# Performance work log

Hardware: AMD Instinct MI355X
Metric: run time of the kernel (lower is better)

## Reference

```python
import jax, jax.numpy as jnp
import numpy as np

NX, DX, H, DO = 8192, 8, 1024, 1


def setup_inputs() -> dict:
    key = jax.random.key(0)
    ks = jax.random.split(key, 7)
    s1 = 1.0 / np.sqrt(DX)  # torch Linear default init bound
    s2 = 1.0 / np.sqrt(H)
    x = jax.random.normal(ks[0], (NX, DX), jnp.float32)
    W1 = jax.random.uniform(ks[1], (H, DX), jnp.float32, -s1, s1)
    b1 = jax.random.uniform(ks[2], (H,), jnp.float32, -s1, s1)
    W2 = jax.random.uniform(ks[3], (H, H), jnp.float32, -s2, s2)
    b2 = jax.random.uniform(ks[4], (H,), jnp.float32, -s2, s2)
    W3 = jax.random.uniform(ks[5], (DO, H), jnp.float32, -s2, s2)
    b3 = jax.random.uniform(ks[6], (DO,), jnp.float32, -s2, s2)
    return {"x": x, "W1": W1, "b1": b1, "W2": W2, "b2": b2, "W3": W3, "b3": b3}


def reference(x, W1, b1, W2, b2, W3, b3):
    # Forward: Linear -> Tanh -> Linear -> Tanh -> Linear
    z1 = jnp.tanh(x @ W1.T + b1)          # [nx, h]
    z2 = jnp.tanh(z1 @ W2.T + b2)         # [nx, h]
    y = z2 @ W3.T + b3                    # [nx, out]

    # DerivTanh(h) = 4/(e^-h + e^h)^2 = sech^2(h) = 1 - tanh(h)^2
    d1 = 1.0 - z1 * z1                    # [nx, h]
    d2 = 1.0 - z2 * z2                    # [nx, h]

    # Vectorized analytic Jacobian (original loops over each input dim k):
    # tmp_k = d2 * (W2 @ (d1 * W1[:, k]))  then  dydx_k = W3 @ tmp_k
    J = d1[:, :, None] * W1[None, :, :]                    # [nx, h, dx]
    J = d2[:, :, None] * jnp.einsum('ij,njk->nik', W2, J)  # [nx, h, dx]
    dydx = jnp.einsum('oj,njk->nok', W3, J)                # [nx, out, dx]
    # Match original list-of-dx ordering: dydx[k] has shape [nx, out]
    dydx = jnp.transpose(dydx, (2, 0, 1))                  # [dx, nx, out]
    return y, dydx
```

## Files before the change

kernel.cpp:

```cpp
#include <hip/hip_runtime.h>
#include <stdint.h>

#define NXS 8192
#define HS  1024

typedef __attribute__((ext_vector_type(8))) short short8;
typedef __attribute__((ext_vector_type(4))) float f32x4;

__device__ __forceinline__ float bf2f(uint32_t b) {
    union { uint32_t u; float f; } c; c.u = b << 16; return c.f;
}
__device__ __forceinline__ uint16_t f2bf(float f) {
    union { float f; uint32_t u; } c; c.f = f;
    return (uint16_t)((c.u + 0x7fffu + ((c.u >> 16) & 1u)) >> 16);
}


__global__ __launch_bounds__(256) void k01(
    const float* __restrict__ x, const float* __restrict__ W1,
    const float* __restrict__ b1, const float* __restrict__ W2,
    const float* __restrict__ b3, uint16_t* __restrict__ Z1p,
    uint16_t* __restrict__ Bp1, uint16_t* __restrict__ Bp2,
    uint16_t* __restrict__ W1T, float* __restrict__ out)
{
    const int b = blockIdx.x, t = threadIdx.x;
    if (b < 512) {
        __shared__ float w1s[8192];
        __shared__ float b1s[1024];
        __shared__ float xs[16][8];
        const int rt = b;
#pragma unroll
        for (int i = 0; i < 8; ++i)
            *(float4*)&w1s[(i * 256 + t) * 4] = *(const float4*)(W1 + (i * 256 + t) * 4);
#pragma unroll
        for (int i = 0; i < 4; ++i) b1s[i * 256 + t] = b1[i * 256 + t];
        if (t < 128) xs[t >> 3][t & 7] = x[rt * 128 + t];
        __syncthreads();
        const int r = t & 15;
        float xv[8];
#pragma unroll
        for (int k = 0; k < 8; ++k) xv[k] = xs[r][k];
#pragma unroll
        for (int c8 = 0; c8 < 8; ++c8) {
            const int kb = (t >> 4) + c8 * 16;
            uint16_t o[8];
#pragma unroll
            for (int j = 0; j < 8; ++j) {
                const int col = kb * 8 + j;
                float s = b1s[col];
#pragma unroll
                for (int k = 0; k < 8; ++k) s += xv[k] * w1s[col * 8 + k];
                o[j] = f2bf(tanhf(s));
            }
            const int c = kb >> 2, lq = kb & 3;
            uint16_t* dst = Z1p + ((size_t)(rt * 32 + c) * 64 + lq * 16 + r) * 8;
            *(ushort4*)dst       = *(ushort4*)&o[0];
            *(ushort4*)(dst + 4) = *(ushort4*)&o[4];
        }
    } else if (b < 1024) {
        const int tid = (b - 512) * 256 + t;
        const int l = tid & 63, c = (tid >> 6) & 31, g = tid >> 11;
        const int lr = l & 15, lq = l >> 4;
        const float* src = W2 + (size_t)(g * 16 + lr) * HS + c * 32 + lq * 8;
        float4 a0 = *(const float4*)src;
        float4 a1 = *(const float4*)(src + 4);
        uint16_t o[8];
        o[0] = f2bf(a0.x); o[1] = f2bf(a0.y); o[2] = f2bf(a0.z); o[3] = f2bf(a0.w);
        o[4] = f2bf(a1.x); o[5] = f2bf(a1.y); o[6] = f2bf(a1.z); o[7] = f2bf(a1.w);
        *(ushort4*)(Bp1 + (size_t)tid * 8)     = *(ushort4*)&o[0];
        *(ushort4*)(Bp1 + (size_t)tid * 8 + 4) = *(ushort4*)&o[4];
    } else if (b < 1536) {
        const int tid = (b - 1024) * 256 + t;
        const int l = tid & 63, c = (tid >> 6) & 31, g = tid >> 11;
        const int lr = l & 15, lq = l >> 4;
        uint16_t o[8];
#pragma unroll
        for (int j2 = 0; j2 < 8; ++j2)
            o[j2] = f2bf(W2[(size_t)(c * 32 + lq * 8 + j2) * HS + g * 16 + lr]);
        *(ushort4*)(Bp2 + (size_t)tid * 8)     = *(ushort4*)&o[0];
        *(ushort4*)(Bp2 + (size_t)tid * 8 + 4) = *(ushort4*)&o[4];
    } else if (b < 1824) {
        const int idx = (b - 1536) * 256 + t;
        out[idx] = (idx < NXS) ? b3[0] : 0.f;
    } else {
        const int idx = (b - 1824) * 256 + t;
        const int r = idx >> 10, cc = idx & 1023;
        W1T[idx] = (r < 8) ? f2bf(W1[cc * 8 + r]) : (uint16_t)0;
    }
}

template <int MODE>
__global__ __launch_bounds__(256, 4) void gemm_k(
    const uint16_t* __restrict__ Ap, const uint16_t* __restrict__ Bp,
    const float* __restrict__ bias, const float* __restrict__ W3,
    uint16_t* __restrict__ Vp, float* __restrict__ yOut,
    const uint16_t* __restrict__ Z1p, const uint16_t* __restrict__ W1T,
    float* __restrict__ dOut)
{
    __shared__ __attribute__((aligned(16))) uint16_t smem[64 * 136];
    const int t = threadIdx.x;
    const int wave = t >> 6, lane = t & 63;
    const int lq = lane >> 4, lr = lane & 15;
    const int rowBase = blockIdx.x * 64;
    const int colBase = blockIdx.y * 128;

    const uint16_t* pA  = Ap + ((size_t)(rowBase >> 4) * 32) * 512 + (size_t)lane * 8;
    const uint16_t* pB0 = Bp + ((size_t)(colBase >> 4) + wave * 2) * 16384 + (size_t)lane * 8;
    const uint16_t* pB1 = pB0 + 16384;

    f32x4 acc[4][2] = {};

    short8 ac[4], b0c, b1c;
#pragma unroll
    for (int ti = 0; ti < 4; ++ti)
        ac[ti] = *(const short8*)(pA + (size_t)ti * 16384);
    b0c = *(const short8*)pB0;
    b1c = *(const short8*)pB1;

    for (int c = 0; c < 32; ++c) {
        short8 an[4] = {ac[0], ac[1], ac[2], ac[3]};
        short8 b0n = b0c, b1n = b1c;
        if (c < 31) {
            const size_t off = (size_t)(c + 1) * 512;
#pragma unroll
            for (int ti = 0; ti < 4; ++ti)
                an[ti] = *(const short8*)(pA + (size_t)ti * 16384 + off);
            b0n = *(const short8*)(pB0 + off);
            b1n = *(const short8*)(pB1 + off);
        }
#pragma unroll
        for (int ti = 0; ti < 4; ++ti) {
            acc[ti][0] = __builtin_amdgcn_mfma_f32_16x16x32_bf16(ac[ti], b0c, acc[ti][0], 0, 0, 0);
            acc[ti][1] = __builtin_amdgcn_mfma_f32_16x16x32_bf16(ac[ti], b1c, acc[ti][1], 0, 0, 0);
        }
#pragma unroll
        for (int ti = 0; ti < 4; ++ti) ac[ti] = an[ti];
        b0c = b0n; b1c = b1n;
    }

    if (MODE == 0) {
        float cB[2], cW[2]; int cCol[2];
#pragma unroll
        for (int tj = 0; tj < 2; ++tj) {
            cCol[tj] = wave * 32 + tj * 16 + lr;
            cB[tj] = bias[colBase + cCol[tj]];
            cW[tj] = W3[colBase + cCol[tj]];
        }
#pragma unroll
        for (int ti = 0; ti < 4; ++ti) {
#pragma unroll
            for (int r = 0; r < 4; ++r) {
                int rowl = ti * 16 + lq * 4 + r;
                float ys = 0.f;
#pragma unroll
                for (int tj = 0; tj < 2; ++tj) {
                    float z2 = tanhf(acc[ti][tj][r] + cB[tj]);
                    ys += z2 * cW[tj];
                    smem[rowl * 136 + cCol[tj]] = f2bf((1.f - z2 * z2) * cW[tj]);
                }
                ys += __shfl_xor(ys, 1); ys += __shfl_xor(ys, 2);
                ys += __shfl_xor(ys, 4); ys += __shfl_xor(ys, 8);
                if (lr == 0) atomicAdd(&yOut[rowBase + rowl], ys);
            }
        }
        __syncthreads();
#pragma unroll
        for (int i = 0; i < 4; ++i) {
            const int s = i * 256 + t;
            const int rl = s >> 4, kc = s & 15;
            short8 v = *(const short8*)(smem + rl * 136 + kc * 8);
            const int rt = (rowBase >> 4) + (rl >> 4);
            const int c2 = (colBase >> 5) + (kc >> 2);
            *(short8*)(Vp + ((size_t)(rt * 32 + c2) * 64 + (kc & 3) * 16 + (rl & 15)) * 8) = v;
        }
    } else {
#pragma unroll
        for (int ti = 0; ti < 4; ++ti)
#pragma unroll
            for (int r = 0; r < 4; ++r) {
                const int rowl = ti * 16 + lq * 4 + r;
                const int rt_z = (rowBase >> 4) + ti;
                const int lrp = lq * 4 + r;
#pragma unroll
                for (int tj = 0; tj < 2; ++tj) {
                    const int col = colBase + wave * 32 + tj * 16 + lr;
                    const int cz = col >> 5, lqz = (col >> 3) & 3, jz = col & 7;
                    float z1 = bf2f(Z1p[((size_t)(rt_z * 32 + cz) * 64 + lqz * 16 + lrp) * 8 + jz]);
                    smem[rowl * 136 + wave * 32 + tj * 16 + lr] =
                        f2bf(acc[ti][tj][r] * (1.f - z1 * z1));
                }
            }
        __syncthreads();
        f32x4 dd = {};
#pragma unroll
        for (int kb = 0; kb < 4; ++kb) {
            short8 aF = *(const short8*)(smem + (wave * 16 + lr) * 136 + kb * 32 + lq * 8);
            short8 bF = *(const short8*)(W1T + lr * HS + colBase + kb * 32 + lq * 8);
            dd = __builtin_amdgcn_mfma_f32_16x16x32_bf16(aF, bF, dd, 0, 0, 0);
        }
        if (lr < 8) {
            const int row = rowBase + wave * 16 + lq * 4;
#pragma unroll
            for (int rg = 0; rg < 4; ++rg)
                atomicAdd(&dOut[(size_t)lr * NXS + row + rg], dd[rg]);
        }
    }
}

extern "C" void kernel_launch(void* const* d_in, const int* in_sizes, int n_in,
                              void* d_out, int out_size, void* d_ws, size_t ws_size,
                              hipStream_t stream) {
    (void)in_sizes; (void)n_in; (void)out_size; (void)ws_size;
    const float* x  = (const float*)d_in[0];
    const float* W1 = (const float*)d_in[1];
    const float* b1 = (const float*)d_in[2];
    const float* W2 = (const float*)d_in[3];
    const float* b2 = (const float*)d_in[4];
    const float* W3 = (const float*)d_in[5];
    const float* b3 = (const float*)d_in[6];
    float* out = (float*)d_out;

    char* ws = (char*)d_ws;
    uint16_t* Z1p = (uint16_t*)(ws);
    uint16_t* Vp  = (uint16_t*)(ws + (size_t)16 * 1024 * 1024);
    uint16_t* Bp1 = (uint16_t*)(ws + (size_t)32 * 1024 * 1024);
    uint16_t* Bp2 = (uint16_t*)(ws + (size_t)34 * 1024 * 1024);
    uint16_t* W1T = (uint16_t*)(ws + (size_t)36 * 1024 * 1024);

    k01<<<1888, 256, 0, stream>>>(x, W1, b1, W2, b3, Z1p, Bp1, Bp2, W1T, out);
    gemm_k<0><<<dim3(NXS / 64, HS / 128), 256, 0, stream>>>(
        Z1p, Bp1, b2, W3, Vp, out, nullptr, nullptr, nullptr);
    gemm_k<1><<<dim3(NXS / 64, HS / 128), 256, 0, stream>>>(
        Vp, Bp2, nullptr, nullptr, nullptr, nullptr, Z1p, W1T, out + NXS);
}
```

Before: 154.1 us.

## Stage A tiles through LDS with async global-to-LDS triple buffering

The A operand is no longer loaded redundantly by each of the four waves straight from global memory. Each block now copies it once per step into a three-slot LDS ring using global_load_lds, which all waves then read. The B fragments stay in registers with two k-chunks prefetched per iteration, and there is one barrier per iteration. This cuts A global traffic roughly fourfold at the cost of LDS reads and a sync each step. The ring reuse depends on barrier ordering and async-copy completion, which is a correctness risk.

```diff
diff --git a/kernel.cpp b/kernel.cpp
--- a/kernel.cpp
+++ b/kernel.cpp
@@ -13,6 +13,12 @@
 __device__ __forceinline__ uint16_t f2bf(float f) {
     union { float f; uint32_t u; } c; c.f = f;
     return (uint16_t)((c.u + 0x7fffu + ((c.u >> 16) & 1u)) >> 16);
+}
+__device__ __forceinline__ void async_cp16(const void* g, void* l) {
+    __builtin_amdgcn_global_load_lds(
+        (const __attribute__((address_space(1))) void*)g,
+        (__attribute__((address_space(3))) void*)l,
+        16, 0, 0);
 }
 
 
@@ -97,46 +103,62 @@
     const uint16_t* __restrict__ Z1p, const uint16_t* __restrict__ W1T,
     float* __restrict__ dOut)
 {
-    __shared__ __attribute__((aligned(16))) uint16_t smem[64 * 136];
+    __shared__ __attribute__((aligned(16))) uint16_t smem[12288];
     const int t = threadIdx.x;
     const int wave = t >> 6, lane = t & 63;
     const int lq = lane >> 4, lr = lane & 15;
     const int rowBase = blockIdx.x * 64;
     const int colBase = blockIdx.y * 128;
 
-    const uint16_t* pA  = Ap + ((size_t)(rowBase >> 4) * 32) * 512 + (size_t)lane * 8;
+    const int ti0 = t >> 7, cp = (t >> 6) & 1, ln = t & 63;
+    const uint16_t* gA0 = Ap + (((size_t)(rowBase >> 4) + ti0) * 32 + cp) * 512 + (size_t)ln * 8;
+    const uint16_t* gA1 = Ap + (((size_t)(rowBase >> 4) + ti0 + 2) * 32 + cp) * 512 + (size_t)ln * 8;
     const uint16_t* pB0 = Bp + ((size_t)(colBase >> 4) + wave * 2) * 16384 + (size_t)lane * 8;
     const uint16_t* pB1 = pB0 + 16384;
 
     f32x4 acc[4][2] = {};
 
-    short8 ac[4], b0c, b1c;
-#pragma unroll
-    for (int ti = 0; ti < 4; ++ti)
-        ac[ti] = *(const short8*)(pA + (size_t)ti * 16384);
-    b0c = *(const short8*)pB0;
-    b1c = *(const short8*)pB1;
-
-    for (int c = 0; c < 32; ++c) {
-        short8 an[4] = {ac[0], ac[1], ac[2], ac[3]};
-        short8 b0n = b0c, b1n = b1c;
-        if (c < 31) {
-            const size_t off = (size_t)(c + 1) * 512;
+    async_cp16(gA0, (char*)smem + t * 16);
+    async_cp16(gA1, (char*)smem + 4096 + t * 16);
+    short8 bc00 = *(const short8*)pB0;
+    short8 bc01 = *(const short8*)pB1;
+    short8 bc10 = *(const short8*)(pB0 + 512);
+    short8 bc11 = *(const short8*)(pB1 + 512);
+
+    int buf = 0;
+    for (int it = 0; it < 16; ++it) {
+        short8 bn00 = bc00, bn01 = bc01, bn10 = bc10, bn11 = bc11;
+        const int nb = (buf == 2) ? 0 : buf + 1;
+        if (it < 15) {
+            const size_t aoff = (size_t)(it + 1) * 1024;
+            async_cp16(gA0 + aoff, (char*)smem + nb * 8192 + t * 16);
+            async_cp16(gA1 + aoff, (char*)smem + nb * 8192 + 4096 + t * 16);
+            const size_t boff = (size_t)(2 * it + 2) * 512;
+            bn00 = *(const short8*)(pB0 + boff);
+            bn01 = *(const short8*)(pB1 + boff);
+            bn10 = *(const short8*)(pB0 + boff + 512);
+            bn11 = *(const short8*)(pB1 + boff + 512);
+        }
+        __syncthreads();
+        const short* pA = (const short*)smem + buf * 4096;
+#pragma unroll
+        for (int kk = 0; kk < 2; ++kk) {
+            short8 af[4];
 #pragma unroll
             for (int ti = 0; ti < 4; ++ti)
-                an[ti] = *(const short8*)(pA + (size_t)ti * 16384 + off);
-            b0n = *(const short8*)(pB0 + off);
-            b1n = *(const short8*)(pB1 + off);
-        }
-#pragma unroll
-        for (int ti = 0; ti < 4; ++ti) {
-            acc[ti][0] = __builtin_amdgcn_mfma_f32_16x16x32_bf16(ac[ti], b0c, acc[ti][0], 0, 0, 0);
-            acc[ti][1] = __builtin_amdgcn_mfma_f32_16x16x32_bf16(ac[ti], b1c, acc[ti][1], 0, 0, 0);
-        }
-#pragma unroll
-        for (int ti = 0; ti < 4; ++ti) ac[ti] = an[ti];
-        b0c = b0n; b1c = b1n;
+                af[ti] = *(const short8*)(pA + ti * 1024 + kk * 512 + lane * 8);
+            const short8 b0 = kk ? bc10 : bc00;
+            const short8 b1 = kk ? bc11 : bc01;
+#pragma unroll
+            for (int ti = 0; ti < 4; ++ti) {
+                acc[ti][0] = __builtin_amdgcn_mfma_f32_16x16x32_bf16(af[ti], b0, acc[ti][0], 0, 0, 0);
+                acc[ti][1] = __builtin_amdgcn_mfma_f32_16x16x32_bf16(af[ti], b1, acc[ti][1], 0, 0, 0);
+            }
+        }
+        bc00 = bn00; bc01 = bn01; bc10 = bn10; bc11 = bn11;
+        buf = nb;
     }
+    __syncthreads();
 
     if (MODE == 0) {
         float cB[2], cW[2]; int cCol[2];
```

Result: faster. 137.0 us (-11.1%).

## Stage A tiles in LDS via async copy with 2x2 wave layout

Applied to the files above, without the earlier changes.

The GEMM main loop now loads the shared A row-tile into LDS once per block, using global_load_lds async copies in a triple-buffered ring. Previously every wave read all four A fragments from global memory itself. Waves are rearranged into a 2x2 grid, each computing a 32x64 sub-tile, so A fragments are reused from LDS and each wave reads four B fragments. This cuts redundant global A traffic but adds a __syncthreads per K iteration and more B register pressure.

```diff
diff --git a/kernel.cpp b/kernel.cpp
--- a/kernel.cpp
+++ b/kernel.cpp
@@ -13,6 +13,12 @@
 __device__ __forceinline__ uint16_t f2bf(float f) {
     union { float f; uint32_t u; } c; c.f = f;
     return (uint16_t)((c.u + 0x7fffu + ((c.u >> 16) & 1u)) >> 16);
+}
+__device__ __forceinline__ void async_cp16(const void* g, void* l) {
+    __builtin_amdgcn_global_load_lds(
+        (const __attribute__((address_space(1))) void*)g,
+        (__attribute__((address_space(3))) void*)l,
+        16, 0, 0);
 }
 
 
@@ -97,63 +103,73 @@
     const uint16_t* __restrict__ Z1p, const uint16_t* __restrict__ W1T,
     float* __restrict__ dOut)
 {
-    __shared__ __attribute__((aligned(16))) uint16_t smem[64 * 136];
+    __shared__ __attribute__((aligned(16))) uint16_t smem[8704];
     const int t = threadIdx.x;
     const int wave = t >> 6, lane = t & 63;
     const int lq = lane >> 4, lr = lane & 15;
+    const int wm = wave >> 1, wn = wave & 1;
     const int rowBase = blockIdx.x * 64;
     const int colBase = blockIdx.y * 128;
 
-    const uint16_t* pA  = Ap + ((size_t)(rowBase >> 4) * 32) * 512 + (size_t)lane * 8;
-    const uint16_t* pB0 = Bp + ((size_t)(colBase >> 4) + wave * 2) * 16384 + (size_t)lane * 8;
-    const uint16_t* pB1 = pB0 + 16384;
-
-    f32x4 acc[4][2] = {};
-
-    short8 ac[4], b0c, b1c;
-#pragma unroll
-    for (int ti = 0; ti < 4; ++ti)
-        ac[ti] = *(const short8*)(pA + (size_t)ti * 16384);
-    b0c = *(const short8*)pB0;
-    b1c = *(const short8*)pB1;
-
-    for (int c = 0; c < 32; ++c) {
-        short8 an[4] = {ac[0], ac[1], ac[2], ac[3]};
-        short8 b0n = b0c, b1n = b1c;
-        if (c < 31) {
-            const size_t off = (size_t)(c + 1) * 512;
-#pragma unroll
-            for (int ti = 0; ti < 4; ++ti)
-                an[ti] = *(const short8*)(pA + (size_t)ti * 16384 + off);
-            b0n = *(const short8*)(pB0 + off);
-            b1n = *(const short8*)(pB1 + off);
-        }
-#pragma unroll
-        for (int ti = 0; ti < 4; ++ti) {
-            acc[ti][0] = __builtin_amdgcn_mfma_f32_16x16x32_bf16(ac[ti], b0c, acc[ti][0], 0, 0, 0);
-            acc[ti][1] = __builtin_amdgcn_mfma_f32_16x16x32_bf16(ac[ti], b1c, acc[ti][1], 0, 0, 0);
-        }
-#pragma unroll
-        for (int ti = 0; ti < 4; ++ti) ac[ti] = an[ti];
-        b0c = b0n; b1c = b1n;
+    const uint16_t* gA = Ap + ((size_t)((rowBase >> 4) + (t >> 6)) * 32) * 512
+                            + (size_t)(t & 63) * 8;
+    const uint16_t* pB[4];
+#pragma unroll
+    for (int tj = 0; tj < 4; ++tj)
+        pB[tj] = Bp + ((size_t)(colBase >> 4) + wn * 4 + tj) * 16384 + (size_t)lane * 8;
+
+    f32x4 acc[2][4] = {};
+
+    async_cp16(gA, (char*)smem + t * 16);
+    short8 bc[4];
+#pragma unroll
+    for (int tj = 0; tj < 4; ++tj) bc[tj] = *(const short8*)pB[tj];
+
+    int buf = 0;
+    for (int it = 0; it < 32; ++it) {
+        short8 bn[4] = {bc[0], bc[1], bc[2], bc[3]};
+        const int nb = (buf == 2) ? 0 : buf + 1;
+        if (it < 31) {
+            async_cp16(gA + (size_t)(it + 1) * 512, (char*)smem + nb * 4096 + t * 16);
+            const size_t boff = (size_t)(it + 1) * 512;
+#pragma unroll
+            for (int tj = 0; tj < 4; ++tj)
+                bn[tj] = *(const short8*)(pB[tj] + boff);
+        }
+        __syncthreads();
+        const short* pA = (const short*)smem + buf * 2048;
+        short8 af[2];
+#pragma unroll
+        for (int ti = 0; ti < 2; ++ti)
+            af[ti] = *(const short8*)(pA + (wm * 2 + ti) * 512 + lane * 8);
+#pragma unroll
+        for (int ti = 0; ti < 2; ++ti)
+#pragma unroll
+            for (int tj = 0; tj < 4; ++tj)
+                acc[ti][tj] = __builtin_amdgcn_mfma_f32_16x16x32_bf16(
+                    af[ti], bc[tj], acc[ti][tj], 0, 0, 0);
+#pragma unroll
+        for (int tj = 0; tj < 4; ++tj) bc[tj] = bn[tj];
+        buf = nb;
     }
+    __syncthreads();
 
     if (MODE == 0) {
-        float cB[2], cW[2]; int cCol[2];
-#pragma unroll
-        for (int tj = 0; tj < 2; ++tj) {
-            cCol[tj] = wave * 32 + tj * 16 + lr;
+        float cB[4], cW[4]; int cCol[4];
+#pragma unroll
+        for (int tj = 0; tj < 4; ++tj) {
+            cCol[tj] = wn * 64 + tj * 16 + lr;
             cB[tj] = bias[colBase + cCol[tj]];
             cW[tj] = W3[colBase + cCol[tj]];
         }
 #pragma unroll
-        for (int ti = 0; ti < 4; ++ti) {
+        for (int ti = 0; ti < 2; ++ti) {
 #pragma unroll
             for (int r = 0; r < 4; ++r) {
-                int rowl = ti * 16 + lq * 4 + r;
+                int rowl = wm * 32 + ti * 16 + lq * 4 + r;
                 float ys = 0.f;
 #pragma unroll
-                for (int tj = 0; tj < 2; ++tj) {
+                for (int tj = 0; tj < 4; ++tj) {
                     float z2 = tanhf(acc[ti][tj][r] + cB[tj]);
                     ys += z2 * cW[tj];
                     smem[rowl * 136 + cCol[tj]] = f2bf((1.f - z2 * z2) * cW[tj]);
@@ -175,18 +191,18 @@
         }
     } else {
 #pragma unroll
-        for (int ti = 0; ti < 4; ++ti)
+        for (int ti = 0; ti < 2; ++ti)
 #pragma unroll
             for (int r = 0; r < 4; ++r) {
-                const int rowl = ti * 16 + lq * 4 + r;
-                const int rt_z = (rowBase >> 4) + ti;
+                const int rowl = wm * 32 + ti * 16 + lq * 4 + r;
+                const int rt_z = (rowBase >> 4) + wm * 2 + ti;
                 const int lrp = lq * 4 + r;
 #pragma unroll
-                for (int tj = 0; tj < 2; ++tj) {
-                    const int col = colBase + wave * 32 + tj * 16 + lr;
+                for (int tj = 0; tj < 4; ++tj) {
+                    const int col = colBase + wn * 64 + tj * 16 + lr;
                     const int cz = col >> 5, lqz = (col >> 3) & 3, jz = col & 7;
                     float z1 = bf2f(Z1p[((size_t)(rt_z * 32 + cz) * 64 + lqz * 16 + lrp) * 8 + jz]);
-                    smem[rowl * 136 + wave * 32 + tj * 16 + lr] =
+                    smem[rowl * 136 + wn * 64 + tj * 16 + lr] =
                         f2bf(acc[ti][tj][r] * (1.f - z1 * z1));
                 }
             }
```

After: 147.7 us. 1.04x faster.
